# Optimization experiments

Measured on AMD Instinct MI355X. Metric: run time of the kernel, lower is better.

## Reference

```python
import jax, jax.numpy as jnp
import numpy as np

H = 12          # num_attention_heads
D = 64          # attention_head_size
HID = H * D     # hidden_size = 768
M = 1024        # max_position_embeddings


def setup_inputs() -> dict:
    key = jax.random.key(0)
    ks = jax.random.split(key, 9)
    B, S = 4, 1024
    s = 0.02
    return {
        "hidden_states": jax.random.normal(ks[0], (B, S, HID), jnp.float32),
        "attention_mask": jnp.zeros((B, 1, 1, S), jnp.float32),
        "Wq": jax.random.normal(ks[1], (HID, HID), jnp.float32) * s,
        "bq": jnp.zeros((HID,), jnp.float32),
        "Wk": jax.random.normal(ks[2], (HID, HID), jnp.float32) * s,
        "bk": jnp.zeros((HID,), jnp.float32),
        "Wv": jax.random.normal(ks[3], (HID, HID), jnp.float32) * s,
        "bv": jnp.zeros((HID,), jnp.float32),
        "dist_emb": jax.random.normal(ks[4], (2 * M - 1, D), jnp.float32) * s,
    }


def reference(hidden_states, attention_mask, Wq, bq, Wk, bk, Wv, bv, dist_emb):
    B, S, _ = hidden_states.shape

    def heads(x):  # [B,S,HID] -> [B,H,S,D]
        return x.reshape(B, S, H, D).transpose(0, 2, 1, 3)

    q = heads(hidden_states @ Wq + bq)
    k = heads(hidden_states @ Wk + bk)
    v = heads(hidden_states @ Wv + bv)

    # raw dot-product scores [B,H,S,S]
    scores = jnp.einsum('bhld,bhrd->bhlr', q, k)

    # relative_key_query positional bias
    pos = jnp.arange(S)
    distance = pos[:, None] - pos[None, :] + (M - 1)   # [S,S] in [0, 2M-2]
    pe = dist_emb[distance]                            # [S,S,D]
    scores = scores + jnp.einsum('bhld,lrd->bhlr', q, pe) \
                    + jnp.einsum('bhrd,lrd->bhlr', k, pe)

    scores = scores / jnp.sqrt(jnp.asarray(D, scores.dtype)) + attention_mask
    probs = jax.nn.softmax(scores, axis=-1)            # dropout is identity in eval

    ctx = jnp.einsum('bhlr,bhrd->bhld', probs, v)      # [B,H,S,D]
    ctx = ctx.transpose(0, 2, 1, 3).reshape(B, S, HID)
    return ctx, probs
```

## Files before the change

kernel.cpp:

```cpp
#include <hip/hip_runtime.h>
#include <hip/hip_bf16.h>

#define DEVFN __device__ __forceinline__

typedef __bf16 bf16x8 __attribute__((ext_vector_type(8)));
typedef float f32x4 __attribute__((ext_vector_type(4)));
typedef unsigned short ushort8 __attribute__((ext_vector_type(8)));
typedef unsigned short us4 __attribute__((ext_vector_type(4)));

namespace {

constexpr int S = 1024;
constexpr int HID = 768;
constexpr int NH = 12;
constexpr int HD = 64;

DEVFN unsigned short f2bf(float f) {
  union { float f; unsigned u; } v; v.f = f;
  unsigned r = v.u + 0x7FFF + ((v.u >> 16) & 1);
  return (unsigned short)(r >> 16);
}

DEVFN float bf2f(unsigned short u) {
  union { unsigned u; float f; } v; v.u = ((unsigned)u) << 16; return v.f;
}

DEVFN f32x4 zero4() { return f32x4{0.f, 0.f, 0.f, 0.f}; }

DEVFN f32x4 mfma_bf16(bf16x8 a, bf16x8 b, f32x4 c) {
  return __builtin_amdgcn_mfma_f32_16x16x32_bf16(a, b, c, 0, 0, 0);
}

DEVFN void gload16(void* lds_base, const void* gsrc) {
  __builtin_amdgcn_global_load_lds(
      (const __attribute__((address_space(1))) void*)gsrc,
      (__attribute__((address_space(3))) void*)lds_base, 16, 0, 0);
}

DEVFN bf16x8 frag_ld(const char* tile, int row, int ch) {
  int chs = ch ^ (row & 7);
  return *(const bf16x8*)(tile + row * 128 + chs * 16);
}

__global__ void k0_cvt_x(const float* __restrict__ x, unsigned short* __restrict__ xb) {
  size_t i = (size_t)(blockIdx.x * 256 + threadIdx.x) * 8;
  float4 a = *(const float4*)(x + i);
  float4 c = *(const float4*)(x + i + 4);
  ushort8 o;
  o[0] = f2bf(a.x); o[1] = f2bf(a.y); o[2] = f2bf(a.z); o[3] = f2bf(a.w);
  o[4] = f2bf(c.x); o[5] = f2bf(c.y); o[6] = f2bf(c.z); o[7] = f2bf(c.w);
  *(ushort8*)(xb + i) = o;
}

__global__ void k0_cvt_pe(const float* __restrict__ de, unsigned short* __restrict__ peb) {
  size_t i = (size_t)(blockIdx.x * 256 + threadIdx.x) * 8;
  int row = (int)(i >> 6);
  ushort8 o;
  if (row < 2047) {
    float4 a = *(const float4*)(de + i);
    float4 c = *(const float4*)(de + i + 4);
    o[0] = f2bf(a.x); o[1] = f2bf(a.y); o[2] = f2bf(a.z); o[3] = f2bf(a.w);
    o[4] = f2bf(c.x); o[5] = f2bf(c.y); o[6] = f2bf(c.z); o[7] = f2bf(c.w);
  } else {
    o = ushort8{0, 0, 0, 0, 0, 0, 0, 0};
  }
  *(ushort8*)(peb + i) = o;
}

__global__ __launch_bounds__(256) void k0_wt(const float* __restrict__ Wq,
                                             const float* __restrict__ Wk,
                                             const float* __restrict__ Wv,
                                             unsigned short* __restrict__ wt) {
  __shared__ float t[64][65];
  int bidx = blockIdx.x;
  int sec = bidx / 144, rem = bidx % 144;
  int ktb = rem / 12, ntb = rem % 12;
  const float* W = (sec == 0) ? Wq : ((sec == 1) ? Wk : Wv);
  int k0 = ktb * 64, n0 = ntb * 64;
  int tid = threadIdx.x;
  #pragma unroll
  for (int p = 0; p < 4; ++p) {
    int id = p * 256 + tid;
    int row = id >> 4, ch = id & 15;
    float4 v = *(const float4*)(W + (size_t)(k0 + row) * 768 + n0 + ch * 4);
    t[row][ch * 4 + 0] = v.x; t[row][ch * 4 + 1] = v.y;
    t[row][ch * 4 + 2] = v.z; t[row][ch * 4 + 3] = v.w;
  }
  __syncthreads();
  #pragma unroll
  for (int p = 0; p < 2; ++p) {
    int id = p * 256 + tid;
    int nrow = id >> 3, c8 = id & 7;
    ushort8 o;
    #pragma unroll
    for (int i = 0; i < 8; ++i) o[i] = f2bf(t[c8 * 8 + i][nrow]);
    *(ushort8*)(wt + (size_t)(sec * 768 + n0 + nrow) * 768 + k0 + c8 * 8) = o;
  }
}

__global__ __launch_bounds__(256) void k1_qkv(
    const unsigned short* __restrict__ xb, const unsigned short* __restrict__ wt,
    const float* __restrict__ bq, const float* __restrict__ bk, const float* __restrict__ bv,
    unsigned short* __restrict__ q_ws, unsigned short* __restrict__ k_ws,
    unsigned short* __restrict__ vt_ws) {
  __shared__ char ldsA[16384], ldsB[16384];
  const int tid = threadIdx.x, lane = tid & 63, wv = tid >> 6;
  const int row16 = lane & 15, cgrp = lane >> 4;
  const int wm = wv >> 1, wn = wv & 1;
  const int ntb = blockIdx.x % 18, mtb = blockIdx.x / 18;
  const int sec = ntb / 6;
  const int n0 = ntb * 128;
  const int m0 = mtb * 128;

  f32x4 acc[4][4];
  #pragma unroll
  for (int i = 0; i < 4; ++i)
    #pragma unroll
    for (int j = 0; j < 4; ++j) acc[i][j] = zero4();

  for (int k0 = 0; k0 < 768; k0 += 64) {
    #pragma unroll
    for (int c = 0; c < 4; ++c) {
      int cc = (wv * 4 + c) * 64 + lane;
      int row = cc >> 3, ch = cc & 7, chs = ch ^ (row & 7);
      gload16(ldsA + (wv * 4 + c) * 1024, xb + (size_t)(m0 + row) * 768 + k0 + chs * 8);
      gload16(ldsB + (wv * 4 + c) * 1024, wt + (size_t)(n0 + row) * 768 + k0 + chs * 8);
    }
    __syncthreads();
    if (sec < 2) {
      bf16x8 bf[4][2];
      #pragma unroll
      for (int nt = 0; nt < 4; ++nt)
        #pragma unroll
        for (int k2 = 0; k2 < 2; ++k2)
          bf[nt][k2] = frag_ld(ldsB, wn * 64 + nt * 16 + row16, k2 * 4 + cgrp);
      #pragma unroll
      for (int mt = 0; mt < 4; ++mt) {
        bf16x8 af0 = frag_ld(ldsA, wm * 64 + mt * 16 + row16, cgrp);
        bf16x8 af1 = frag_ld(ldsA, wm * 64 + mt * 16 + row16, 4 + cgrp);
        #pragma unroll
        for (int nt = 0; nt < 4; ++nt) {
          acc[mt][nt] = mfma_bf16(af0, bf[nt][0], acc[mt][nt]);
          acc[mt][nt] = mfma_bf16(af1, bf[nt][1], acc[mt][nt]);
        }
      }
    } else {
      bf16x8 am[4][2];
      #pragma unroll
      for (int mt = 0; mt < 4; ++mt)
        #pragma unroll
        for (int k2 = 0; k2 < 2; ++k2)
          am[mt][k2] = frag_ld(ldsA, wm * 64 + mt * 16 + row16, k2 * 4 + cgrp);
      #pragma unroll
      for (int nt = 0; nt < 4; ++nt) {
        bf16x8 bv0 = frag_ld(ldsB, wn * 64 + nt * 16 + row16, cgrp);
        bf16x8 bv1 = frag_ld(ldsB, wn * 64 + nt * 16 + row16, 4 + cgrp);
        #pragma unroll
        for (int mt = 0; mt < 4; ++mt) {
          acc[nt][mt] = mfma_bf16(bv0, am[mt][0], acc[nt][mt]);
          acc[nt][mt] = mfma_bf16(bv1, am[mt][1], acc[nt][mt]);
        }
      }
    }
    __syncthreads();
  }

  const int nl0 = (ntb % 6) * 128;
  if (sec < 2) {
    unsigned short* dst = (sec == 0) ? q_ws : k_ws;
    const float* bias = (sec == 0) ? bq : bk;
    #pragma unroll
    for (int nt = 0; nt < 4; ++nt) {
      int nn = nl0 + wn * 64 + nt * 16 + row16;
      float bb = bias[nn];
      int hh = nn >> 6, dd = nn & 63;
      #pragma unroll
      for (int mt = 0; mt < 4; ++mt)
        #pragma unroll
        for (int j = 0; j < 4; ++j) {
          int m = m0 + wm * 64 + mt * 16 + cgrp * 4 + j;
          int b_ = m >> 10, s_ = m & 1023;
          dst[(size_t)((b_ * 12 + hh) * 1024 + s_) * 64 + dd] = f2bf(acc[mt][nt][j] + bb);
        }
    }
  } else {
    #pragma unroll
    for (int nt = 0; nt < 4; ++nt)
      #pragma unroll
      for (int j = 0; j < 4; ++j) {
        int nn = nl0 + wn * 64 + nt * 16 + cgrp * 4 + j;
        float bb = bv[nn];
        int hh = nn >> 6, dd = nn & 63;
        #pragma unroll
        for (int mt = 0; mt < 4; ++mt) {
          int m = m0 + wm * 64 + mt * 16 + row16;
          int b_ = m >> 10, s_ = m & 1023;
          vt_ws[(size_t)((b_ * 12 + hh) * 64 + dd) * 1024 + s_] = f2bf(acc[nt][mt][j] + bb);
        }
      }
  }
}

__global__ __launch_bounds__(256) void k2_score(
    const unsigned short* __restrict__ q_ws, const unsigned short* __restrict__ k_ws,
    const unsigned short* __restrict__ peb, const float* __restrict__ mask,
    unsigned short* __restrict__ p_out, float* __restrict__ rsum_part) {
  __shared__ char k_lds[8192];
  __shared__ char pe_lds[16384];
  __shared__ unsigned short s3t[4][64 * 36];
  __shared__ unsigned short p_sh[64 * 64];
  __shared__ float rsum_sh[2][64];

  const int tid = threadIdx.x, lane = tid & 63, wv = tid >> 6;
  const int wl = wv >> 1, wr = wv & 1;
  const int row16 = lane & 15, cgrp = lane >> 4;

  const int bid = blockIdx.x;
  const int rt = bid & 15, lt = (bid >> 4) & 15, bh = bid >> 8;
  const int b = bh / NH;
  const int l0 = lt * 64, r0 = rt * 64;

  const unsigned short* qh = q_ws + (size_t)bh * S * HD;
  const unsigned short* khp = k_ws + (size_t)bh * S * HD;
  const float* maskb = mask + b * S;

  #pragma unroll
  for (int c = 0; c < 2; ++c) {
    int cc = (wv * 2 + c) * 64 + lane;
    int row = cc >> 3, ch = cc & 7, chs = ch ^ (row & 7);
    gload16(k_lds + (wv * 2 + c) * 1024, khp + (size_t)(r0 + row) * HD + chs * 8);
  }
  {
    int m0 = l0 - r0 + 960;
    #pragma unroll
    for (int c = 0; c < 4; ++c) {
      int cc = (wv * 4 + c) * 64 + lane;
      int row = cc >> 3, ch = cc & 7, chs = ch ^ (row & 7);
      gload16(pe_lds + (wv * 4 + c) * 1024, peb + (size_t)(m0 + row) * HD + chs * 8);
    }
  }

  bf16x8 qf[2][2];
  #pragma unroll
  for (int ltl = 0; ltl < 2; ++ltl)
    #pragma unroll
    for (int k2 = 0; k2 < 2; ++k2)
      qf[ltl][k2] = *(const bf16x8*)(qh + (size_t)(l0 + wl * 32 + ltl * 16 + row16) * HD +
                                     k2 * 32 + cgrp * 8);
  __syncthreads();

  bf16x8 kf[2][2], pef[4][2];
  #pragma unroll
  for (int rtl = 0; rtl < 2; ++rtl)
    #pragma unroll
    for (int k2 = 0; k2 < 2; ++k2)
      kf[rtl][k2] = frag_ld(k_lds, wr * 32 + rtl * 16 + row16, k2 * 4 + cgrp);
  const int qb = (wl - wr) * 32 + 32;
  #pragma unroll
  for (int jt = 0; jt < 4; ++jt)
    #pragma unroll
    for (int k2 = 0; k2 < 2; ++k2)
      pef[jt][k2] = frag_ld(pe_lds, qb + jt * 16 + row16, k2 * 4 + cgrp);

  unsigned short* s3w = &s3t[wv][0];

  #pragma unroll
  for (int rtl = 0; rtl < 2; ++rtl)
    #pragma unroll
    for (int jt = 0; jt < 4; ++jt) {
      f32x4 a3 = zero4();
      a3 = mfma_bf16(kf[rtl][0], pef[jt][0], a3);
      a3 = mfma_bf16(kf[rtl][1], pef[jt][1], a3);
      us4 o;
      o[0] = f2bf(a3[0]); o[1] = f2bf(a3[1]); o[2] = f2bf(a3[2]); o[3] = f2bf(a3[3]);
      *(us4*)(s3w + (jt * 16 + row16) * 36 + rtl * 16 + cgrp * 4) = o;
    }

  f32x4 s1[2][2];
  #pragma unroll
  for (int ltl = 0; ltl < 2; ++ltl)
    #pragma unroll
    for (int rtl = 0; rtl < 2; ++rtl) {
      f32x4 a1 = zero4();
      a1 = mfma_bf16(qf[ltl][0], kf[rtl][0], a1);
      a1 = mfma_bf16(qf[ltl][1], kf[rtl][1], a1);
      s1[ltl][rtl] = a1;
    }
  f32x4 s2[2][4];
  #pragma unroll
  for (int ltl = 0; ltl < 2; ++ltl)
    #pragma unroll
    for (int jt = 0; jt < 4; ++jt) {
      f32x4 a2 = zero4();
      a2 = mfma_bf16(qf[ltl][0], pef[jt][0], a2);
      a2 = mfma_bf16(qf[ltl][1], pef[jt][1], a2);
      s2[ltl][jt] = a2;
    }

  float rs[2][4] = {};
  #pragma unroll
  for (int rtl = 0; rtl < 2; ++rtl) {
    float mval = maskb[r0 + wr * 32 + rtl * 16 + row16];
    #pragma unroll
    for (int ltl = 0; ltl < 2; ++ltl) {
      const int jtA = ltl - rtl + 1;
      #pragma unroll
      for (int j = 0; j < 4; ++j) {
        int dl = ltl * 16 + cgrp * 4 + j;
        int dr = rtl * 16 + row16;
        int jjq = dl - dr + 31;
        int src = (lane & 48) | (jjq & 15);
        float vA = __shfl(s2[ltl][jtA][j], src, 64);
        float vB = __shfl(s2[ltl][jtA + 1][j], src, 64);
        float b1 = ((jjq >> 4) == jtA) ? vA : vB;
        float b2 = bf2f(s3w[jjq * 36 + dr]);
        float logit = (s1[ltl][rtl][j] + b1 + b2) * 0.125f + mval;
        float p = __expf(logit);
        rs[ltl][j] += p;
        int dlb = wl * 32 + dl, drb = wr * 32 + dr;
        p_sh[dlb * 64 + (drb ^ ((dlb & 7) << 3))] = f2bf(p);
      }
    }
  }

  #pragma unroll
  for (int ltl = 0; ltl < 2; ++ltl)
    #pragma unroll
    for (int j = 0; j < 4; ++j) {
      float v = rs[ltl][j];
      v += __shfl_xor(v, 1, 64);
      v += __shfl_xor(v, 2, 64);
      v += __shfl_xor(v, 4, 64);
      v += __shfl_xor(v, 8, 64);
      rs[ltl][j] = v;
    }
  if (row16 == 0) {
    #pragma unroll
    for (int ltl = 0; ltl < 2; ++ltl)
      #pragma unroll
      for (int j = 0; j < 4; ++j)
        rsum_sh[wr][wl * 32 + ltl * 16 + cgrp * 4 + j] = rs[ltl][j];
  }
  __syncthreads();

  if (tid < 64)
    rsum_part[((size_t)(bh * 16 + lt) * 64 + tid) * 16 + rt] =
        rsum_sh[0][tid] + rsum_sh[1][tid];

  #pragma unroll
  for (int p2 = 0; p2 < 2; ++p2) {
    int id = p2 * 256 + tid, dl = id >> 3, c = id & 7;
    uint4 w = *(const uint4*)((const char*)p_sh + dl * 128 + (c ^ (dl & 7)) * 16);
    *(uint4*)(p_out + ((size_t)bh * S + l0 + dl) * S + r0 + c * 8) = w;
  }
}

__global__ __launch_bounds__(256) void k3_pv(
    const unsigned short* __restrict__ p_in, const unsigned short* __restrict__ vt_ws,
    const float* __restrict__ rsum_part, float* __restrict__ ctx_part,
    float* __restrict__ inv_ws, float* __restrict__ out_probs) {
  __shared__ char p_sh[2][8192];
  __shared__ float inv_sh[64];

  const int tid = threadIdx.x, lane = tid & 63, wv = tid >> 6;
  const int row16 = lane & 15, cgrp = lane >> 4;
  const int rq = blockIdx.x & 3, lt = (blockIdx.x >> 2) & 15, bh = blockIdx.x >> 6;
  const int l0 = lt * 64, rbase = rq * 256;

  const unsigned short* vth = vt_ws + (size_t)bh * HD * S;
  float* probs_bh = out_probs + (size_t)bh * S * S;

  if (tid < 64) {
    const float4* pp =
        (const float4*)(rsum_part + ((size_t)(bh * 16 + lt) * 64 + tid) * 16);
    float s = 0.f;
    #pragma unroll
    for (int i = 0; i < 4; ++i) {
      float4 v = pp[i];
      s += v.x + v.y + v.z + v.w;
    }
    float iv = 1.0f / s;
    inv_sh[tid] = iv;
    if (rq == 0) inv_ws[bh * S + l0 + tid] = iv;
  }

  auto stage = [&](char* buf, int r0) {
    #pragma unroll
    for (int c = 0; c < 2; ++c) {
      int cc = (wv * 2 + c) * 64 + lane;
      int row = cc >> 3, ch = cc & 7, chs = ch ^ (row & 7);
      gload16(buf + (wv * 2 + c) * 1024,
              p_in + ((size_t)bh * S + l0 + row) * S + r0 + chs * 8);
    }
  };

  stage(p_sh[0], rbase);
  __syncthreads();

  f32x4 ctxacc[4] = {zero4(), zero4(), zero4(), zero4()};

  for (int it = 0; it < 4; ++it) {
    const int r0 = rbase + it * 64, cur = it & 1;
    if (it < 3) stage(p_sh[cur ^ 1], r0 + 64);
    const char* cb = p_sh[cur];

    #pragma unroll
    for (int p2 = 0; p2 < 2; ++p2) {
      int id = p2 * 256 + tid, dl = id >> 3, c = id & 7;
      uint4 w = *(const uint4*)(cb + dl * 128 + (c ^ (dl & 7)) * 16);
      const unsigned short* pu = (const unsigned short*)&w;
      float iv = inv_sh[dl];
      float* dst = probs_bh + (size_t)(l0 + dl) * S + r0 + c * 8;
      float4 lo{bf2f(pu[0]) * iv, bf2f(pu[1]) * iv, bf2f(pu[2]) * iv, bf2f(pu[3]) * iv};
      float4 hi{bf2f(pu[4]) * iv, bf2f(pu[5]) * iv, bf2f(pu[6]) * iv, bf2f(pu[7]) * iv};
      *(float4*)dst = lo; *(float4*)(dst + 4) = hi;
    }

    {
      int lrow = wv * 16 + row16;
      bf16x8 pa[2];
      #pragma unroll
      for (int kc = 0; kc < 2; ++kc) {
        int ch = kc * 4 + cgrp, chs = ch ^ (lrow & 7);
        pa[kc] = *(const bf16x8*)(cb + lrow * 128 + chs * 16);
      }
      #pragma unroll
      for (int dt = 0; dt < 4; ++dt) {
        bf16x8 vb0 = *(const bf16x8*)(vth + (size_t)(dt * 16 + row16) * S + r0 + cgrp * 8);
        bf16x8 vb1 = *(const bf16x8*)(vth + (size_t)(dt * 16 + row16) * S + r0 + 32 + cgrp * 8);
        ctxacc[dt] = mfma_bf16(pa[0], vb0, ctxacc[dt]);
        ctxacc[dt] = mfma_bf16(pa[1], vb1, ctxacc[dt]);
      }
    }
    __syncthreads();
  }

  #pragma unroll
  for (int dt = 0; dt < 4; ++dt)
    #pragma unroll
    for (int j = 0; j < 4; ++j) {
      int lr = wv * 16 + cgrp * 4 + j;
      ctx_part[((size_t)(rq * 48 + bh) * S + l0 + lr) * 64 + dt * 16 + row16] =
          ctxacc[dt][j];
    }
}

__global__ __launch_bounds__(256) void k4_red(
    const float* __restrict__ ctx_part, const float* __restrict__ inv_ws,
    float* __restrict__ out_ctx) {
  int gid = blockIdx.x * 256 + threadIdx.x;
  int t = gid >> 3, d0 = (gid & 7) * 8;
  int bh = t >> 10, l = t & 1023;
  float4 s0{0.f, 0.f, 0.f, 0.f}, s1{0.f, 0.f, 0.f, 0.f};
  #pragma unroll
  for (int rq = 0; rq < 4; ++rq) {
    const float* p = ctx_part + ((size_t)(rq * 48 + bh) * S + l) * 64 + d0;
    float4 a = *(const float4*)p;
    float4 b = *(const float4*)(p + 4);
    s0.x += a.x; s0.y += a.y; s0.z += a.z; s0.w += a.w;
    s1.x += b.x; s1.y += b.y; s1.z += b.z; s1.w += b.w;
  }
  float iv = inv_ws[t];
  s0.x *= iv; s0.y *= iv; s0.z *= iv; s0.w *= iv;
  s1.x *= iv; s1.y *= iv; s1.z *= iv; s1.w *= iv;
  int b_ = bh / NH, h = bh % NH;
  float* dst = out_ctx + ((size_t)(b_ * S + l)) * HID + h * HD + d0;
  *(float4*)dst = s0;
  *(float4*)(dst + 4) = s1;
}

}

extern "C" void kernel_launch(void* const* d_in, const int* in_sizes, int n_in,
                              void* d_out, int out_size, void* d_ws, size_t ws_size,
                              hipStream_t stream) {
  const float* hidden = (const float*)d_in[0];
  const float* mask   = (const float*)d_in[1];
  const float* Wq = (const float*)d_in[2];
  const float* bq = (const float*)d_in[3];
  const float* Wk = (const float*)d_in[4];
  const float* bk = (const float*)d_in[5];
  const float* Wv = (const float*)d_in[6];
  const float* bv = (const float*)d_in[7];
  const float* de = (const float*)d_in[8];

  unsigned short* ws = (unsigned short*)d_ws;
  unsigned short* q_ws  = ws;
  unsigned short* k_ws  = ws + 3145728;
  unsigned short* vt_ws = ws + 6291456;
  unsigned short* xb    = ws + 9437184;
  unsigned short* wt    = ws + 12582912;
  unsigned short* peb   = ws + 14352384;
  float* rsum_part = (float*)(ws + 14483456);
  unsigned short* p_ws  = ws + 16056320;
  float* ctx_part = (float*)(ws + 66387968);
  float* inv_ws   = (float*)(ws + 91553792);

  float* outc = (float*)d_out;
  float* outp = outc + (size_t)4 * 1024 * 768;

  hipLaunchKernelGGL(k0_cvt_x, dim3(1536), dim3(256), 0, stream, hidden, xb);
  hipLaunchKernelGGL(k0_cvt_pe, dim3(64), dim3(256), 0, stream, de, peb);
  hipLaunchKernelGGL(k0_wt, dim3(432), dim3(256), 0, stream, Wq, Wk, Wv, wt);
  hipLaunchKernelGGL(k1_qkv, dim3(576), dim3(256), 0, stream,
                     xb, wt, bq, bk, bv, q_ws, k_ws, vt_ws);
  hipLaunchKernelGGL(k2_score, dim3(12288), dim3(256), 0, stream,
                     q_ws, k_ws, peb, mask, p_ws, rsum_part);
  hipLaunchKernelGGL(k3_pv, dim3(3072), dim3(256), 0, stream,
                     p_ws, vt_ws, rsum_part, ctx_part, inv_ws, outp);
  hipLaunchKernelGGL(k4_red, dim3(1536), dim3(256), 0, stream,
                     ctx_part, inv_ws, outc);
}
```

Measured before the change: 238.7 us.

## Shrink QKV tiles, alias score-kernel LDS, and swizzle block order for XCD locality

The QKV projection GEMM moves from 128x128 tiles to 64x64 tiles (2304 blocks instead of 576), with smaller accumulators and LDS, to fill more CUs. The score kernel now reuses the K/PE shared buffer for the s3 scratch after an extra barrier, which lowers LDS use and may raise occupancy. Both the score and PV kernels remap block IDs with a modulo-8 swizzle so that neighbouring tiles of the same head go to the same XCD and share its L2. Smaller GEMM tiles lower data reuse per block, and the extra barrier adds some synchronisation cost.

```diff
diff --git a/kernel.cpp b/kernel.cpp
--- a/kernel.cpp
+++ b/kernel.cpp
@@ -103,101 +103,81 @@
     const float* __restrict__ bq, const float* __restrict__ bk, const float* __restrict__ bv,
     unsigned short* __restrict__ q_ws, unsigned short* __restrict__ k_ws,
     unsigned short* __restrict__ vt_ws) {
-  __shared__ char ldsA[16384], ldsB[16384];
+  __shared__ char ldsA[8192], ldsB[8192];
   const int tid = threadIdx.x, lane = tid & 63, wv = tid >> 6;
   const int row16 = lane & 15, cgrp = lane >> 4;
-  const int wm = wv >> 1, wn = wv & 1;
-  const int ntb = blockIdx.x % 18, mtb = blockIdx.x / 18;
-  const int sec = ntb / 6;
-  const int n0 = ntb * 128;
-  const int m0 = mtb * 128;
-
-  f32x4 acc[4][4];
-  #pragma unroll
-  for (int i = 0; i < 4; ++i)
-    #pragma unroll
-    for (int j = 0; j < 4; ++j) acc[i][j] = zero4();
+  const int ntb = blockIdx.x % 36, mtb = blockIdx.x / 36;
+  const int sec = ntb / 12;
+  const int n0 = ntb * 64;
+  const int m0 = mtb * 64;
+
+  f32x4 acc[4] = {zero4(), zero4(), zero4(), zero4()};
 
   for (int k0 = 0; k0 < 768; k0 += 64) {
     #pragma unroll
-    for (int c = 0; c < 4; ++c) {
-      int cc = (wv * 4 + c) * 64 + lane;
+    for (int c = 0; c < 2; ++c) {
+      int cc = (wv * 2 + c) * 64 + lane;
       int row = cc >> 3, ch = cc & 7, chs = ch ^ (row & 7);
-      gload16(ldsA + (wv * 4 + c) * 1024, xb + (size_t)(m0 + row) * 768 + k0 + chs * 8);
-      gload16(ldsB + (wv * 4 + c) * 1024, wt + (size_t)(n0 + row) * 768 + k0 + chs * 8);
+      gload16(ldsA + (wv * 2 + c) * 1024, xb + (size_t)(m0 + row) * 768 + k0 + chs * 8);
+      gload16(ldsB + (wv * 2 + c) * 1024, wt + (size_t)(n0 + row) * 768 + k0 + chs * 8);
     }
     __syncthreads();
     if (sec < 2) {
-      bf16x8 bf[4][2];
+      bf16x8 af[2];
+      #pragma unroll
+      for (int k2 = 0; k2 < 2; ++k2) af[k2] = frag_ld(ldsA, wv * 16 + row16, k2 * 4 + cgrp);
       #pragma unroll
       for (int nt = 0; nt < 4; ++nt)
         #pragma unroll
-        for (int k2 = 0; k2 < 2; ++k2)
-          bf[nt][k2] = frag_ld(ldsB, wn * 64 + nt * 16 + row16, k2 * 4 + cgrp);
-      #pragma unroll
-      for (int mt = 0; mt < 4; ++mt) {
-        bf16x8 af0 = frag_ld(ldsA, wm * 64 + mt * 16 + row16, cgrp);
-        bf16x8 af1 = frag_ld(ldsA, wm * 64 + mt * 16 + row16, 4 + cgrp);
-        #pragma unroll
-        for (int nt = 0; nt < 4; ++nt) {
-          acc[mt][nt] = mfma_bf16(af0, bf[nt][0], acc[mt][nt]);
-          acc[mt][nt] = mfma_bf16(af1, bf[nt][1], acc[mt][nt]);
+        for (int k2 = 0; k2 < 2; ++k2) {
+          bf16x8 bf = frag_ld(ldsB, nt * 16 + row16, k2 * 4 + cgrp);
+          acc[nt] = mfma_bf16(af[k2], bf, acc[nt]);
         }
-      }
     } else {
-      bf16x8 am[4][2];
+      bf16x8 af[2];
+      #pragma unroll
+      for (int k2 = 0; k2 < 2; ++k2) af[k2] = frag_ld(ldsB, wv * 16 + row16, k2 * 4 + cgrp);
       #pragma unroll
       for (int mt = 0; mt < 4; ++mt)
         #pragma unroll
-        for (int k2 = 0; k2 < 2; ++k2)
-          am[mt][k2] = frag_ld(ldsA, wm * 64 + mt * 16 + row16, k2 * 4 + cgrp);
-      #pragma unroll
-      for (int nt = 0; nt < 4; ++nt) {
-        bf16x8 bv0 = frag_ld(ldsB, wn * 64 + nt * 16 + row16, cgrp);
-        bf16x8 bv1 = frag_ld(ldsB, wn * 64 + nt * 16 + row16, 4 + cgrp);
-        #pragma unroll
-        for (int mt = 0; mt < 4; ++mt) {
-          acc[nt][mt] = mfma_bf16(bv0, am[mt][0], acc[nt][mt]);
-          acc[nt][mt] = mfma_bf16(bv1, am[mt][1], acc[nt][mt]);
+        for (int k2 = 0; k2 < 2; ++k2) {
+          bf16x8 bx = frag_ld(ldsA, mt * 16 + row16, k2 * 4 + cgrp);
+          acc[mt] = mfma_bf16(af[k2], bx, acc[mt]);
         }
-      }
     }
     __syncthreads();
   }
 
-  const int nl0 = (ntb % 6) * 128;
   if (sec < 2) {
     unsigned short* dst = (sec == 0) ? q_ws : k_ws;
     const float* bias = (sec == 0) ? bq : bk;
+    int nl0 = (ntb % 12) * 64;
     #pragma unroll
     for (int nt = 0; nt < 4; ++nt) {
-      int nn = nl0 + wn * 64 + nt * 16 + row16;
+      int nn = nl0 + nt * 16 + row16;
       float bb = bias[nn];
       int hh = nn >> 6, dd = nn & 63;
       #pragma unroll
-      for (int mt = 0; mt < 4; ++mt)
-        #pragma unroll
-        for (int j = 0; j < 4; ++j) {
-          int m = m0 + wm * 64 + mt * 16 + cgrp * 4 + j;
-          int b_ = m >> 10, s_ = m & 1023;
-          dst[(size_t)((b_ * 12 + hh) * 1024 + s_) * 64 + dd] = f2bf(acc[mt][nt][j] + bb);
-        }
+      for (int j = 0; j < 4; ++j) {
+        int m = m0 + wv * 16 + cgrp * 4 + j;
+        int b_ = m >> 10, s_ = m & 1023;
+        dst[(size_t)((b_ * 12 + hh) * 1024 + s_) * 64 + dd] = f2bf(acc[nt][j] + bb);
+      }
     }
   } else {
-    #pragma unroll
-    for (int nt = 0; nt < 4; ++nt)
-      #pragma unroll
-      for (int j = 0; j < 4; ++j) {
-        int nn = nl0 + wn * 64 + nt * 16 + cgrp * 4 + j;
-        float bb = bv[nn];
-        int hh = nn >> 6, dd = nn & 63;
-        #pragma unroll
-        for (int mt = 0; mt < 4; ++mt) {
-          int m = m0 + wm * 64 + mt * 16 + row16;
-          int b_ = m >> 10, s_ = m & 1023;
-          vt_ws[(size_t)((b_ * 12 + hh) * 64 + dd) * 1024 + s_] = f2bf(acc[nt][mt][j] + bb);
-        }
+    int nl0 = (ntb % 12) * 64;
+    #pragma unroll
+    for (int j = 0; j < 4; ++j) {
+      int nn = nl0 + wv * 16 + cgrp * 4 + j;
+      float bb = bv[nn];
+      int hh = nn >> 6, dd = nn & 63;
+      #pragma unroll
+      for (int mt = 0; mt < 4; ++mt) {
+        int m = m0 + mt * 16 + row16;
+        int b_ = m >> 10, s_ = m & 1023;
+        vt_ws[(size_t)((b_ * 12 + hh) * 64 + dd) * 1024 + s_] = f2bf(acc[mt][j] + bb);
       }
+    }
   }
 }
 
@@ -205,18 +185,20 @@
     const unsigned short* __restrict__ q_ws, const unsigned short* __restrict__ k_ws,
     const unsigned short* __restrict__ peb, const float* __restrict__ mask,
     unsigned short* __restrict__ p_out, float* __restrict__ rsum_part) {
-  __shared__ char k_lds[8192];
-  __shared__ char pe_lds[16384];
-  __shared__ unsigned short s3t[4][64 * 36];
+  __shared__ __align__(16) char kpe_lds[24576];
   __shared__ unsigned short p_sh[64 * 64];
   __shared__ float rsum_sh[2][64];
+
+  char* k_lds = kpe_lds;
+  char* pe_lds = kpe_lds + 8192;
 
   const int tid = threadIdx.x, lane = tid & 63, wv = tid >> 6;
   const int wl = wv >> 1, wr = wv & 1;
   const int row16 = lane & 15, cgrp = lane >> 4;
 
   const int bid = blockIdx.x;
-  const int rt = bid & 15, lt = (bid >> 4) & 15, bh = bid >> 8;
+  const int swz = (bid & 7) * 1536 + (bid >> 3);
+  const int rt = swz & 15, lt = (swz >> 4) & 15, bh = swz >> 8;
   const int b = bh / NH;
   const int l0 = lt * 64, r0 = rt * 64;
 
@@ -261,8 +243,9 @@
     #pragma unroll
     for (int k2 = 0; k2 < 2; ++k2)
       pef[jt][k2] = frag_ld(pe_lds, qb + jt * 16 + row16, k2 * 4 + cgrp);
-
-  unsigned short* s3w = &s3t[wv][0];
+  __syncthreads();
+
+  unsigned short* s3w = (unsigned short*)kpe_lds + wv * (64 * 36);
 
   #pragma unroll
   for (int rtl = 0; rtl < 2; ++rtl)
@@ -364,7 +347,9 @@
 
   const int tid = threadIdx.x, lane = tid & 63, wv = tid >> 6;
   const int row16 = lane & 15, cgrp = lane >> 4;
-  const int rq = blockIdx.x & 3, lt = (blockIdx.x >> 2) & 15, bh = blockIdx.x >> 6;
+  const int bid = blockIdx.x;
+  const int swz = (bid & 7) * 384 + (bid >> 3);
+  const int rq = swz & 3, lt = (swz >> 2) & 15, bh = swz >> 6;
   const int l0 = lt * 64, rbase = rq * 256;
 
   const unsigned short* vth = vt_ws + (size_t)bh * HD * S;
@@ -502,7 +487,7 @@
   hipLaunchKernelGGL(k0_cvt_x, dim3(1536), dim3(256), 0, stream, hidden, xb);
   hipLaunchKernelGGL(k0_cvt_pe, dim3(64), dim3(256), 0, stream, de, peb);
   hipLaunchKernelGGL(k0_wt, dim3(432), dim3(256), 0, stream, Wq, Wk, Wv, wt);
-  hipLaunchKernelGGL(k1_qkv, dim3(576), dim3(256), 0, stream,
+  hipLaunchKernelGGL(k1_qkv, dim3(2304), dim3(256), 0, stream,
                      xb, wt, bq, bk, bv, q_ws, k_ws, vt_ws);
   hipLaunchKernelGGL(k2_score, dim3(12288), dim3(256), 0, stream,
                      q_ws, k_ws, peb, mask, p_ws, rsum_part);
```

New measurement: 230.2 us. 3.5% less time.
